# Kernel optimization log

Measured on AMD Instinct MI355X. Metric: run time of the kernel, lower is better.

Reference implementation:

```python
import jax, jax.numpy as jnp
import numpy as np

N, F, O = 8192, 1024, 1024
NUM_NEIGH = 10


def setup_inputs() -> dict:
    key = jax.random.key(0)
    k1, k2, k3, k4, k5 = jax.random.split(key, 5)
    X = jax.random.normal(k1, (N, F), dtype=jnp.float32)
    A = jax.random.uniform(k2, (N, N), dtype=jnp.float32)
    stdv = 1.0 / np.sqrt(O)
    W = jax.random.uniform(k3, (2 * F, O), dtype=jnp.float32, minval=-stdv, maxval=stdv)
    b = jax.random.uniform(k4, (O,), dtype=jnp.float32, minval=-stdv, maxval=stdv)
    # Uniform neighbor sampling (original uses np.random.choice over range(N) per node)
    sampled_idx = jax.random.randint(k5, (N, NUM_NEIGH), 0, N, dtype=jnp.int32)
    return {"X": X, "A": A, "W": W, "b": b, "sampled_idx": sampled_idx}


def reference(X, A, W, b, sampled_idx):
    # aggregate: mean of uniformly sampled neighbor features per node.
    # (The matrix_power of the normalized A in the original is dead code; A's
    #  values never influence the output.)
    gathered = X[sampled_idx]                 # [N, num_neigh, F]
    aggregated = jnp.mean(gathered, axis=1)   # [N, F]
    combined = jnp.concatenate([X, aggregated], axis=1)  # [N, 2F]
    return combined @ W + b                   # [N, O]
```

## Files before the change

kernel.cpp:

```cpp
#include <hip/hip_runtime.h>
#include <stdint.h>

#define NN 8192
#define FD 1024
#define OD 1024
#define KD 2048
#define NB 10

typedef short bf16x8 __attribute__((ext_vector_type(8)));
typedef float f32x4  __attribute__((ext_vector_type(4)));

static __device__ __forceinline__ ushort f2bf(float f) {
  union { float f; uint32_t i; } v; v.f = f;
  uint32_t x = v.i;
  return (ushort)((x + 0x7FFFu + ((x >> 16) & 1u)) >> 16);
}

static __device__ __forceinline__ void async16(const ushort* g, ushort* l) {
  __builtin_amdgcn_global_load_lds(
      (const __attribute__((address_space(1))) uint32_t*)(const void*)g,
      (__attribute__((address_space(3))) uint32_t*)(void*)l, 16, 0, 0);
}

__global__ __launch_bounds__(256) void agg_f32(const float* __restrict__ X,
                                               const int* __restrict__ idx,
                                               ushort* __restrict__ aggb) {
  const int row = blockIdx.x;
  const int c4  = threadIdx.x;
  const int* ip = idx + (size_t)row * NB;
  int nb[NB];
#pragma unroll
  for (int j = 0; j < NB; ++j) nb[j] = ip[j];
  float4 acc = make_float4(0.f, 0.f, 0.f, 0.f);
#pragma unroll
  for (int j = 0; j < NB; ++j) {
    const float4 v = *reinterpret_cast<const float4*>(X + (size_t)nb[j] * FD + c4 * 4);
    acc.x += v.x; acc.y += v.y; acc.z += v.z; acc.w += v.w;
  }
  ushort o[4];
  o[0] = f2bf(acc.x * 0.1f); o[1] = f2bf(acc.y * 0.1f);
  o[2] = f2bf(acc.z * 0.1f); o[3] = f2bf(acc.w * 0.1f);
  *reinterpret_cast<uint2*>(aggb + (size_t)row * FD + c4 * 4) =
      *reinterpret_cast<const uint2*>(o);
}

__global__ __launch_bounds__(1024) void wconv(const float* __restrict__ W,
                                              ushort* __restrict__ Wtb) {
  __shared__ float tile[64][65];
  const int k0 = blockIdx.x * 64;
  const int n0 = blockIdx.y * 64;
  const int tx = threadIdx.x;
  const int ty = threadIdx.y;
#pragma unroll
  for (int r = 0; r < 4; ++r) {
    const int kl = ty + r * 16;
    tile[kl][tx] = W[(size_t)(k0 + kl) * OD + n0 + tx];
  }
  __syncthreads();
#pragma unroll
  for (int r = 0; r < 4; ++r) {
    const int nl = ty + r * 16;
    Wtb[(size_t)(n0 + nl) * KD + k0 + tx] = f2bf(tile[tx][nl]);
  }
}

__global__ __launch_bounds__(256, 2) void gemm_fast(const float* __restrict__ X,
                                                    const ushort* __restrict__ aggb,
                                                    const ushort* __restrict__ Wtb,
                                                    const float* __restrict__ Bias,
                                                    float* __restrict__ Out) {
  __shared__ ushort lA[128 * 32];
  __shared__ ushort lB[128 * 32];
  const int t    = threadIdx.x;
  const int m0   = blockIdx.y * 128;
  const int n0   = blockIdx.x * 128;
  const int wave = t >> 6;
  const int lane = t & 63;
  const int wm   = (wave & 1) * 64;
  const int wn   = (wave >> 1) * 64;
  const int l15  = lane & 15;
  const int quad = lane >> 4;

  f32x4 acc[4][4];
#pragma unroll
  for (int i = 0; i < 4; ++i)
#pragma unroll
    for (int j = 0; j < 4; ++j) acc[i][j] = (f32x4){0.f, 0.f, 0.f, 0.f};

  for (int kt = 0; kt < KD / 32; ++kt) {
    const int k0 = kt * 32;
#pragma unroll
    for (int r = 0; r < 2; ++r) {
      const int q = r * 256 + t;
      const int row = q >> 2, ch = q & 3;
      async16(Wtb + (size_t)(n0 + row) * KD + k0 + ch * 8, lB + q * 8);
    }
    if (k0 < FD) {
#pragma unroll
      for (int r = 0; r < 2; ++r) {
        const int q = r * 256 + t;
        const int row = q >> 2, ch = q & 3;
        const float* p = X + (size_t)(m0 + row) * FD + k0 + ch * 8;
        const float4 a = *reinterpret_cast<const float4*>(p);
        const float4 b = *reinterpret_cast<const float4*>(p + 4);
        bf16x8 v;
        v[0] = (short)f2bf(a.x); v[1] = (short)f2bf(a.y);
        v[2] = (short)f2bf(a.z); v[3] = (short)f2bf(a.w);
        v[4] = (short)f2bf(b.x); v[5] = (short)f2bf(b.y);
        v[6] = (short)f2bf(b.z); v[7] = (short)f2bf(b.w);
        *reinterpret_cast<bf16x8*>(lA + q * 8) = v;
      }
    } else {
      const int kc = k0 - FD;
#pragma unroll
      for (int r = 0; r < 2; ++r) {
        const int q = r * 256 + t;
        const int row = q >> 2, ch = q & 3;
        async16(aggb + (size_t)(m0 + row) * FD + kc + ch * 8, lA + q * 8);
      }
    }
    __syncthreads();

    bf16x8 afr[4], bfr[4];
#pragma unroll
    for (int mi = 0; mi < 4; ++mi)
      afr[mi] = *reinterpret_cast<const bf16x8*>(lA + (wm + mi * 16 + l15) * 32 + quad * 8);
#pragma unroll
    for (int ni = 0; ni < 4; ++ni)
      bfr[ni] = *reinterpret_cast<const bf16x8*>(lB + (wn + ni * 16 + l15) * 32 + quad * 8);
#pragma unroll
    for (int mi = 0; mi < 4; ++mi)
#pragma unroll
      for (int ni = 0; ni < 4; ++ni)
        acc[mi][ni] = __builtin_amdgcn_mfma_f32_16x16x32_bf16(afr[mi], bfr[ni], acc[mi][ni], 0, 0, 0);
    __syncthreads();
  }

#pragma unroll
  for (int ni = 0; ni < 4; ++ni) {
    const int gn = n0 + wn + ni * 16 + l15;
    const float bv = Bias[gn];
#pragma unroll
    for (int mi = 0; mi < 4; ++mi) {
      const int gm = m0 + wm + mi * 16 + quad * 4;
#pragma unroll
      for (int r = 0; r < 4; ++r)
        Out[(size_t)(gm + r) * OD + gn] = acc[mi][ni][r] + bv;
    }
  }
}

__global__ __launch_bounds__(256) void gemm_fused(const float* __restrict__ X,
                                                  const float* __restrict__ W,
                                                  const float* __restrict__ Bias,
                                                  const int* __restrict__ idx,
                                                  float* __restrict__ Out) {
  __shared__ ushort lA[128 * 32];
  __shared__ ushort lB[32 * 128];
  const int t    = threadIdx.x;
  const int m0   = blockIdx.y * 128;
  const int n0   = blockIdx.x * 128;
  const int wave = t >> 6;
  const int lane = t & 63;
  const int wm   = (wave & 1) * 64;
  const int wn   = (wave >> 1) * 64;
  const int l15  = lane & 15;
  const int quad = lane >> 4;

  f32x4 acc[4][4];
#pragma unroll
  for (int i = 0; i < 4; ++i)
#pragma unroll
    for (int j = 0; j < 4; ++j) acc[i][j] = (f32x4){0.f, 0.f, 0.f, 0.f};

  for (int kt = 0; kt < KD / 32; ++kt) {
    const int k0 = kt * 32;
    if (k0 < FD) {
#pragma unroll
      for (int r = 0; r < 2; ++r) {
        const int q = r * 256 + t;
        const int row = q >> 2, ch = q & 3;
        const float* p = X + (size_t)(m0 + row) * FD + k0 + ch * 8;
        const float4 a = *(const float4*)p;
        const float4 b = *(const float4*)(p + 4);
        bf16x8 v;
        v[0] = (short)f2bf(a.x); v[1] = (short)f2bf(a.y);
        v[2] = (short)f2bf(a.z); v[3] = (short)f2bf(a.w);
        v[4] = (short)f2bf(b.x); v[5] = (short)f2bf(b.y);
        v[6] = (short)f2bf(b.z); v[7] = (short)f2bf(b.w);
        *reinterpret_cast<bf16x8*>(lA + q * 8) = v;
      }
    } else {
      const int kc = k0 - FD;
#pragma unroll
      for (int r = 0; r < 2; ++r) {
        const int q = r * 256 + t;
        const int row = q >> 2, ch = q & 3;
        float a8[8] = {0.f, 0.f, 0.f, 0.f, 0.f, 0.f, 0.f, 0.f};
        const int* ip = idx + (size_t)(m0 + row) * NB;
#pragma unroll
        for (int j = 0; j < NB; ++j) {
          const float* p = X + (size_t)ip[j] * FD + kc + ch * 8;
          const float4 a = *(const float4*)p;
          const float4 b = *(const float4*)(p + 4);
          a8[0] += a.x; a8[1] += a.y; a8[2] += a.z; a8[3] += a.w;
          a8[4] += b.x; a8[5] += b.y; a8[6] += b.z; a8[7] += b.w;
        }
        bf16x8 v;
#pragma unroll
        for (int e = 0; e < 8; ++e) v[e] = (short)f2bf(a8[e] * 0.1f);
        *reinterpret_cast<bf16x8*>(lA + q * 8) = v;
      }
    }
#pragma unroll
    for (int r = 0; r < 2; ++r) {
      const int q = r * 256 + t;
      const int kr = q >> 4, ch = q & 15;
      const float* p = W + (size_t)(k0 + kr) * OD + n0 + ch * 8;
      const float4 a = *(const float4*)p;
      const float4 b = *(const float4*)(p + 4);
      bf16x8 v;
      v[0] = (short)f2bf(a.x); v[1] = (short)f2bf(a.y);
      v[2] = (short)f2bf(a.z); v[3] = (short)f2bf(a.w);
      v[4] = (short)f2bf(b.x); v[5] = (short)f2bf(b.y);
      v[6] = (short)f2bf(b.z); v[7] = (short)f2bf(b.w);
      *reinterpret_cast<bf16x8*>(lB + q * 8) = v;
    }
    __syncthreads();

    bf16x8 afr[4], bfr[4];
#pragma unroll
    for (int mi = 0; mi < 4; ++mi)
      afr[mi] = *reinterpret_cast<const bf16x8*>(lA + (wm + mi * 16 + l15) * 32 + quad * 8);
#pragma unroll
    for (int ni = 0; ni < 4; ++ni) {
      const int col = wn + ni * 16 + l15;
#pragma unroll
      for (int j = 0; j < 8; ++j)
        bfr[ni][j] = (short)lB[(quad * 8 + j) * 128 + col];
    }
#pragma unroll
    for (int mi = 0; mi < 4; ++mi)
#pragma unroll
      for (int ni = 0; ni < 4; ++ni)
        acc[mi][ni] = __builtin_amdgcn_mfma_f32_16x16x32_bf16(afr[mi], bfr[ni], acc[mi][ni], 0, 0, 0);
    __syncthreads();
  }
#pragma unroll
  for (int ni = 0; ni < 4; ++ni) {
    const int gn = n0 + wn + ni * 16 + l15;
    const float bv = Bias[gn];
#pragma unroll
    for (int mi = 0; mi < 4; ++mi) {
      const int gm = m0 + wm + mi * 16 + quad * 4;
#pragma unroll
      for (int r = 0; r < 4; ++r)
        Out[(size_t)(gm + r) * OD + gn] = acc[mi][ni][r] + bv;
    }
  }
}

extern "C" void kernel_launch(void* const* d_in, const int* in_sizes, int n_in,
                              void* d_out, int out_size, void* d_ws, size_t ws_size,
                              hipStream_t stream) {
  const float* X   = (const float*)d_in[0];
  const float* W   = (const float*)d_in[2];
  const float* b   = (const float*)d_in[3];
  const int*   idx = (const int*)d_in[4];
  float* out = (float*)d_out;

  const size_t need = ((size_t)NN * FD + (size_t)OD * KD) * sizeof(ushort);
  if (ws_size >= need) {
    ushort* aggb = (ushort*)d_ws;
    ushort* Wtb  = aggb + (size_t)NN * FD;

    agg_f32<<<NN, 256, 0, stream>>>(X, idx, aggb);
    wconv<<<dim3(KD / 64, OD / 64), dim3(64, 16), 0, stream>>>(W, Wtb);
    gemm_fast<<<dim3(OD / 128, NN / 128), 256, 0, stream>>>(X, aggb, Wtb, b, out);
  } else {
    gemm_fused<<<dim3(OD / 128, NN / 128), 256, 0, stream>>>(X, W, b, idx, out);
  }
}
```

Baseline: 423.8 us.

## Pre-convert X to bf16 in a combined buffer and gather from bf16

A new kernel first converts X to bf16 and writes it into the left half of a combined [N, 2F] bf16 buffer. The neighbor aggregation then gathers from that bf16 copy instead of fp32 X, which halves gather bytes, and writes the mean into the right half. The GEMM now streams both operands with async global-to-LDS loads over the single contiguous K range, dropping the per-tile fp32 conversion and the branch between halves. In exchange there is an extra conversion pass and a larger workspace, and neighbor sums are now taken from bf16-rounded X values.

Result: faster. 402.4 us (-5.1%).

```diff
diff --git a/kernel.cpp b/kernel.cpp
--- a/kernel.cpp
+++ b/kernel.cpp
@@ -10,11 +10,24 @@
 typedef short bf16x8 __attribute__((ext_vector_type(8)));
 typedef float f32x4  __attribute__((ext_vector_type(4)));
 
+static __device__ __forceinline__ float bf2f(ushort u) {
+  union { uint32_t i; float f; } v; v.i = ((uint32_t)u) << 16; return v.f;
+}
 static __device__ __forceinline__ ushort f2bf(float f) {
   union { float f; uint32_t i; } v; v.f = f;
   uint32_t x = v.i;
   return (ushort)((x + 0x7FFFu + ((x >> 16) & 1u)) >> 16);
 }
+static __device__ __forceinline__ bf16x8 cvt8(const float* p) {
+  const float4 a = *reinterpret_cast<const float4*>(p);
+  const float4 b = *reinterpret_cast<const float4*>(p + 4);
+  bf16x8 v;
+  v[0] = (short)f2bf(a.x); v[1] = (short)f2bf(a.y);
+  v[2] = (short)f2bf(a.z); v[3] = (short)f2bf(a.w);
+  v[4] = (short)f2bf(b.x); v[5] = (short)f2bf(b.y);
+  v[6] = (short)f2bf(b.z); v[7] = (short)f2bf(b.w);
+  return v;
+}
 
 static __device__ __forceinline__ void async16(const ushort* g, ushort* l) {
   __builtin_amdgcn_global_load_lds(
@@ -22,26 +35,36 @@
       (__attribute__((address_space(3))) uint32_t*)(void*)l, 16, 0, 0);
 }
 
-__global__ __launch_bounds__(256) void agg_f32(const float* __restrict__ X,
-                                               const int* __restrict__ idx,
-                                               ushort* __restrict__ aggb) {
-  const int row = blockIdx.x;
-  const int c4  = threadIdx.x;
+__global__ __launch_bounds__(256) void xconv(const float* __restrict__ X,
+                                             ushort* __restrict__ Ab) {
+  const int q   = blockIdx.x * 256 + threadIdx.x;
+  const int row = q >> 7;
+  const int col = (q & 127) * 8;
+  const bf16x8 v = cvt8(X + (size_t)row * FD + col);
+  *reinterpret_cast<bf16x8*>(Ab + (size_t)row * KD + col) = v;
+}
+
+__global__ __launch_bounds__(256) void aggk(const int* __restrict__ idx,
+                                            ushort* __restrict__ Ab) {
+  const int row  = blockIdx.x * 2 + (threadIdx.x >> 7);
+  const int lane = threadIdx.x & 127;
+  const int col  = lane * 8;
   const int* ip = idx + (size_t)row * NB;
   int nb[NB];
 #pragma unroll
   for (int j = 0; j < NB; ++j) nb[j] = ip[j];
-  float4 acc = make_float4(0.f, 0.f, 0.f, 0.f);
+  float acc[8] = {0.f, 0.f, 0.f, 0.f, 0.f, 0.f, 0.f, 0.f};
 #pragma unroll
   for (int j = 0; j < NB; ++j) {
-    const float4 v = *reinterpret_cast<const float4*>(X + (size_t)nb[j] * FD + c4 * 4);
-    acc.x += v.x; acc.y += v.y; acc.z += v.z; acc.w += v.w;
-  }
-  ushort o[4];
-  o[0] = f2bf(acc.x * 0.1f); o[1] = f2bf(acc.y * 0.1f);
-  o[2] = f2bf(acc.z * 0.1f); o[3] = f2bf(acc.w * 0.1f);
-  *reinterpret_cast<uint2*>(aggb + (size_t)row * FD + c4 * 4) =
-      *reinterpret_cast<const uint2*>(o);
+    const uint4 v = *reinterpret_cast<const uint4*>(Ab + (size_t)nb[j] * KD + col);
+    const ushort* u = reinterpret_cast<const ushort*>(&v);
+#pragma unroll
+    for (int e = 0; e < 8; ++e) acc[e] += bf2f(u[e]);
+  }
+  bf16x8 o;
+#pragma unroll
+  for (int e = 0; e < 8; ++e) o[e] = (short)f2bf(acc[e] * 0.1f);
+  *reinterpret_cast<bf16x8*>(Ab + (size_t)row * KD + FD + col) = o;
 }
 
 __global__ __launch_bounds__(1024) void wconv(const float* __restrict__ W,
@@ -64,11 +87,10 @@
   }
 }
 
-__global__ __launch_bounds__(256, 2) void gemm_fast(const float* __restrict__ X,
-                                                    const ushort* __restrict__ aggb,
-                                                    const ushort* __restrict__ Wtb,
-                                                    const float* __restrict__ Bias,
-                                                    float* __restrict__ Out) {
+__global__ __launch_bounds__(256, 2) void gemm_fast2(const ushort* __restrict__ Ab,
+                                                     const ushort* __restrict__ Wtb,
+                                                     const float* __restrict__ Bias,
+                                                     float* __restrict__ Out) {
   __shared__ ushort lA[128 * 32];
   __shared__ ushort lB[128 * 32];
   const int t    = threadIdx.x;
@@ -87,38 +109,18 @@
 #pragma unroll
     for (int j = 0; j < 4; ++j) acc[i][j] = (f32x4){0.f, 0.f, 0.f, 0.f};
 
-  for (int kt = 0; kt < KD / 32; ++kt) {
-    const int k0 = kt * 32;
-#pragma unroll
-    for (int r = 0; r < 2; ++r) {
-      const int q = r * 256 + t;
-      const int row = q >> 2, ch = q & 3;
-      async16(Wtb + (size_t)(n0 + row) * KD + k0 + ch * 8, lB + q * 8);
-    }
-    if (k0 < FD) {
-#pragma unroll
-      for (int r = 0; r < 2; ++r) {
-        const int q = r * 256 + t;
-        const int row = q >> 2, ch = q & 3;
-        const float* p = X + (size_t)(m0 + row) * FD + k0 + ch * 8;
-        const float4 a = *reinterpret_cast<const float4*>(p);
-        const float4 b = *reinterpret_cast<const float4*>(p + 4);
-        bf16x8 v;
-        v[0] = (short)f2bf(a.x); v[1] = (short)f2bf(a.y);
-        v[2] = (short)f2bf(a.z); v[3] = (short)f2bf(a.w);
-        v[4] = (short)f2bf(b.x); v[5] = (short)f2bf(b.y);
-        v[6] = (short)f2bf(b.z); v[7] = (short)f2bf(b.w);
-        *reinterpret_cast<bf16x8*>(lA + q * 8) = v;
-      }
-    } else {
-      const int kc = k0 - FD;
-#pragma unroll
-      for (int r = 0; r < 2; ++r) {
-        const int q = r * 256 + t;
-        const int row = q >> 2, ch = q & 3;
-        async16(aggb + (size_t)(m0 + row) * FD + kc + ch * 8, lA + q * 8);
-      }
-    }
+  const int row0 = t >> 2, ch = t & 3;
+  const int row1 = (256 + t) >> 2;
+  const ushort* gA0 = Ab  + (size_t)(m0 + row0) * KD + ch * 8;
+  const ushort* gA1 = Ab  + (size_t)(m0 + row1) * KD + ch * 8;
+  const ushort* gB0 = Wtb + (size_t)(n0 + row0) * KD + ch * 8;
+  const ushort* gB1 = Wtb + (size_t)(n0 + row1) * KD + ch * 8;
+
+  for (int k0 = 0; k0 < KD; k0 += 32) {
+    async16(gA0 + k0, lA + t * 8);
+    async16(gA1 + k0, lA + (256 + t) * 8);
+    async16(gB0 + k0, lB + t * 8);
+    async16(gB1 + k0, lB + (256 + t) * 8);
     __syncthreads();
 
     bf16x8 afr[4], bfr[4];
@@ -180,15 +182,8 @@
       for (int r = 0; r < 2; ++r) {
         const int q = r * 256 + t;
         const int row = q >> 2, ch = q & 3;
-        const float* p = X + (size_t)(m0 + row) * FD + k0 + ch * 8;
-        const float4 a = *(const float4*)p;
-        const float4 b = *(const float4*)(p + 4);
-        bf16x8 v;
-        v[0] = (short)f2bf(a.x); v[1] = (short)f2bf(a.y);
-        v[2] = (short)f2bf(a.z); v[3] = (short)f2bf(a.w);
-        v[4] = (short)f2bf(b.x); v[5] = (short)f2bf(b.y);
-        v[6] = (short)f2bf(b.z); v[7] = (short)f2bf(b.w);
-        *reinterpret_cast<bf16x8*>(lA + q * 8) = v;
+        *reinterpret_cast<bf16x8*>(lA + q * 8) =
+            cvt8(X + (size_t)(m0 + row) * FD + k0 + ch * 8);
       }
     } else {
       const int kc = k0 - FD;
@@ -216,15 +211,8 @@
     for (int r = 0; r < 2; ++r) {
       const int q = r * 256 + t;
       const int kr = q >> 4, ch = q & 15;
-      const float* p = W + (size_t)(k0 + kr) * OD + n0 + ch * 8;
-      const float4 a = *(const float4*)p;
-      const float4 b = *(const float4*)(p + 4);
-      bf16x8 v;
-      v[0] = (short)f2bf(a.x); v[1] = (short)f2bf(a.y);
-      v[2] = (short)f2bf(a.z); v[3] = (short)f2bf(a.w);
-      v[4] = (short)f2bf(b.x); v[5] = (short)f2bf(b.y);
-      v[6] = (short)f2bf(b.z); v[7] = (short)f2bf(b.w);
-      *reinterpret_cast<bf16x8*>(lB + q * 8) = v;
+      *reinterpret_cast<bf16x8*>(lB + q * 8) =
+          cvt8(W + (size_t)(k0 + kr) * OD + n0 + ch * 8);
     }
     __syncthreads();
 
@@ -269,14 +257,15 @@
   const int*   idx = (const int*)d_in[4];
   float* out = (float*)d_out;
 
-  const size_t need = ((size_t)NN * FD + (size_t)OD * KD) * sizeof(ushort);
+  const size_t need = ((size_t)NN * KD + (size_t)OD * KD) * sizeof(ushort);
   if (ws_size >= need) {
-    ushort* aggb = (ushort*)d_ws;
-    ushort* Wtb  = aggb + (size_t)NN * FD;
-
-    agg_f32<<<NN, 256, 0, stream>>>(X, idx, aggb);
+    ushort* Ab  = (ushort*)d_ws;
+    ushort* Wtb = Ab + (size_t)NN * KD;
+
+    xconv<<<NN * FD / (256 * 8), 256, 0, stream>>>(X, Ab);
     wconv<<<dim3(KD / 64, OD / 64), dim3(64, 16), 0, stream>>>(W, Wtb);
-    gemm_fast<<<dim3(OD / 128, NN / 128), 256, 0, stream>>>(X, aggb, Wtb, b, out);
+    aggk<<<NN / 2, 256, 0, stream>>>(idx, Ab);
+    gemm_fast2<<<dim3(OD / 128, NN / 128), 256, 0, stream>>>(Ab, Wtb, b, out);
   } else {
     gemm_fused<<<dim3(OD / 128, NN / 128), 256, 0, stream>>>(X, W, b, idx, out);
   }
```
